# Kernel tuning notes

Measured on AMD Instinct MI355X. Metric: run time of the kernel, lower is better.

## Reference

```python
import jax, jax.numpy as jnp
import numpy as np

N, D, E, L, H, F1, G, A = 4096, 256, 131072, 3, 4, 128, 16, 32

def setup_inputs() -> dict:
    key = jax.random.key(0)
    ks = jax.random.split(key, 12)
    s = lambda k, shape, fan: jax.random.normal(k, shape, jnp.float32) / np.sqrt(fan)
    return {
        "x": jax.random.normal(ks[0], (N, D), jnp.float32),
        "edge_attr": jax.random.uniform(ks[1], (E,), jnp.float32),
        "conv_Wself": s(ks[2], (L, D, D), D),
        "conv_Wnbr": s(ks[3], (L, D, D), D),
        "conv_b": jnp.zeros((L, D), jnp.float32),
        "bn_gamma": jnp.ones((L - 1, D), jnp.float32),
        "bn_beta": jnp.zeros((L - 1, D), jnp.float32),
        "bn_mean": jnp.zeros((L - 1, D), jnp.float32),
        "bn_var": jnp.ones((L - 1, D), jnp.float32),
        "Wqkv": s(ks[4], (3, D, D), D),
        "bqkv": jnp.zeros((3, D), jnp.float32),
        "Wo": s(ks[5], (D, D), D),
        "bo": jnp.zeros((D,), jnp.float32),
        "fc1_W": s(ks[6], (D, F1), D),
        "fc1_b": jnp.zeros((F1,), jnp.float32),
        "AW1": s(ks[7], (G, F1, A), F1),
        "Ab1": jnp.zeros((G, A), jnp.float32),
        "AW2": s(ks[8], (G, A, 1), A),
        "Ab2": jnp.zeros((G, 1), jnp.float32),
        "edge_index": jax.random.randint(ks[9], (2, E), 0, N, jnp.int32),
        "node_groups": jax.random.randint(ks[10], (N,), 0, G, jnp.int32),
    }


def reference(x, edge_attr, conv_Wself, conv_Wnbr, conv_b, bn_gamma, bn_beta,
              bn_mean, bn_var, Wqkv, bqkv, Wo, bo, fc1_W, fc1_b,
              AW1, Ab1, AW2, Ab2, edge_index, node_groups):
    src, dst = edge_index[0], edge_index[1]
    # message-passing conv stack (edge_attr only used by the last, non-attention layer)
    for i in range(L):
        msg = x[src]
        if i == L - 1:
            msg = msg * edge_attr[:, None]
        agg = jax.ops.segment_sum(msg, dst, num_segments=N)
        x = x @ conv_Wself[i] + agg @ conv_Wnbr[i] + conv_b[i]
        if i < L - 1:
            x = bn_gamma[i] * (x - bn_mean[i]) * jax.lax.rsqrt(bn_var[i] + 1e-5) + bn_beta[i]
            x = jax.nn.elu(x)
    # hierarchy self-attention over all N nodes (batch of 1), residual add
    dh = D // H
    q = (x @ Wqkv[0] + bqkv[0]).reshape(N, H, dh)
    k = (x @ Wqkv[1] + bqkv[1]).reshape(N, H, dh)
    v = (x @ Wqkv[2] + bqkv[2]).reshape(N, H, dh)
    scores = jnp.einsum('nhd,mhd->hnm', q, k) / np.sqrt(dh).astype(np.float32)
    attn = jax.nn.softmax(scores, axis=-1)
    o = jnp.einsum('hnm,mhd->nhd', attn, v).reshape(N, D) @ Wo + bo
    x = x + o
    feats = jax.nn.elu(x @ fc1_W + fc1_b)  # [N, F1]; dropout is eval no-op
    # MoE-style per-node group adapter routing: gather tiny MLP weights per node
    h = jax.nn.relu(jnp.einsum('nd,nda->na', feats, AW1[node_groups]) + Ab1[node_groups])
    out = jnp.einsum('na,nao->no', h, AW2[node_groups]) + Ab2[node_groups]  # [N, 1]
    return out
```

## Files before the change

### kernel.cpp

```cpp
#include <hip/hip_runtime.h>
#include <math.h>

#define NN   4096
#define DIM  256
#define NE   131072
#define NH   4
#define DH   64
#define F1D  128
#define NG   16
#define AD   32

typedef unsigned short u16;
typedef unsigned int   u32;
typedef _Float16 f16;
typedef __attribute__((ext_vector_type(8))) _Float16 half8;
typedef __attribute__((ext_vector_type(4))) float f32x4;

enum { EPI_BIAS = 0, EPI_BNELU = 1 };
enum { MEPI_WO = 0, MEPI_FC1 = 1 };

#define MFMA16(a, b, c) __builtin_amdgcn_mfma_f32_16x16x32_f16(a, b, c, 0, 0, 0)

__device__ inline u16 f2h(float x) { union { f16 f; u16 u; } c; c.f = (f16)x; return c.u; }
__device__ inline void split16(float x, u16& h, u16& l) {
    union { f16 f; u16 u; } ch, cl;
    ch.f = (f16)x;
    cl.f = (f16)(x - (float)ch.f);
    h = ch.u; l = cl.u;
}

__global__ void csr_count(const int* __restrict__ dst, int* __restrict__ cnt) {
    int e = blockIdx.x * 256 + threadIdx.x;
    atomicAdd(&cnt[dst[e]], 1);
}

__global__ __launch_bounds__(1024) void csr_scan(
    int* __restrict__ cnt, int* __restrict__ off)
{
    __shared__ int wsum[16];
    const int t = threadIdx.x;
    const int lane = t & 63;
    int4 v = *(const int4*)&cnt[t * 4];
    const int s = v.x + v.y + v.z + v.w;
    int acc = s;
    #pragma unroll
    for (int o = 1; o < 64; o <<= 1) {
        int u = __shfl_up(acc, o);
        if (lane >= o) acc += u;
    }
    if (lane == 63) wsum[t >> 6] = acc;
    __syncthreads();
    if (t < 16) {
        int w0 = wsum[t];
        int a2 = w0;
        #pragma unroll
        for (int o = 1; o < 16; o <<= 1) {
            int u = __shfl_up(a2, o);
            if (t >= o) a2 += u;
        }
        wsum[t] = a2 - w0;
    }
    __syncthreads();
    const int base = wsum[t >> 6] + (acc - s);
    off[t * 4 + 0] = base;
    off[t * 4 + 1] = base + v.x;
    off[t * 4 + 2] = base + v.x + v.y;
    off[t * 4 + 3] = base + v.x + v.y + v.z;
    *(int4*)&cnt[t * 4] = make_int4(0, 0, 0, 0);
    if (t == 1023) off[NN] = base + s;
}

__global__ void csr_fill(const int* __restrict__ dst, const int* __restrict__ src,
                         const float* __restrict__ eattr, const int* __restrict__ off,
                         int* __restrict__ cur, int* __restrict__ esrc,
                         float* __restrict__ ewt) {
    int e = blockIdx.x * 256 + threadIdx.x;
    int d = dst[e];
    int pos = off[d] + atomicAdd(&cur[d], 1);
    esrc[pos] = src[e];
    ewt[pos]  = eattr[e];
}

__global__ __launch_bounds__(256) void prep_kernel(
    const float* __restrict__ x,
    const float* __restrict__ Ws, const float* __restrict__ Wn,
    const float* __restrict__ Wqkv, const float* __restrict__ Wo,
    const float* __restrict__ fc1W,
    u16* __restrict__ xh, u16* __restrict__ xl,
    u16* __restrict__ wch, u16* __restrict__ wcl,
    u16* __restrict__ w4h, u16* __restrict__ w4l,
    u16* __restrict__ f1h, u16* __restrict__ f1l,
    int* __restrict__ cur)
{
    const int b = blockIdx.x;
    const int t = threadIdx.x;
    if (b < 1024) {
        const int gid = b * 256 + t;
        const float4 v = *(const float4*)&x[(size_t)gid * 4];
        u16 h[4], l[4];
        split16(v.x, h[0], l[0]); split16(v.y, h[1], l[1]);
        split16(v.z, h[2], l[2]); split16(v.w, h[3], l[3]);
        *(uint2*)&xh[(size_t)gid * 4] =
            make_uint2((u32)h[0] | ((u32)h[1] << 16), (u32)h[2] | ((u32)h[3] << 16));
        *(uint2*)&xl[(size_t)gid * 4] =
            make_uint2((u32)l[0] | ((u32)l[1] << 16), (u32)l[2] | ((u32)l[3] << 16));
    } else if (b < 1408) {
        const int gid = (b - 1024) * 256 + t;
        const int L = gid / 32768;
        const int rem = gid % 32768;
        const int m = rem / 128;
        const int k4 = (rem % 128) * 4;
        const float* S = Ws + (size_t)L * 65536;
        const float* Nb = Wn + (size_t)L * 65536;
        u16 h[4], l[4];
        #pragma unroll
        for (int j = 0; j < 4; ++j) {
            const int k = k4 + j;
            const float v = (k < 256) ? S[(size_t)k * 256 + m]
                                      : Nb[(size_t)(k - 256) * 256 + m];
            split16(v, h[j], l[j]);
        }
        const size_t o = (size_t)L * 131072 + (size_t)m * 512 + k4;
        *(uint2*)&wch[o] = make_uint2((u32)h[0] | ((u32)h[1] << 16), (u32)h[2] | ((u32)h[3] << 16));
        *(uint2*)&wcl[o] = make_uint2((u32)l[0] | ((u32)l[1] << 16), (u32)l[2] | ((u32)l[3] << 16));
    } else if (b < 1664) {
        const int gid = (b - 1408) * 256 + t;
        const int mat = gid / 16384;
        const int rem = gid % 16384;
        const int m = rem / 64;
        const int k4 = (rem % 64) * 4;
        const float* W = (mat < 3) ? Wqkv + (size_t)mat * 65536 : Wo;
        u16 h[4], l[4];
        #pragma unroll
        for (int j = 0; j < 4; ++j)
            split16(W[(size_t)(k4 + j) * 256 + m], h[j], l[j]);
        const size_t o = (size_t)mat * 65536 + (size_t)m * 256 + k4;
        *(uint2*)&w4h[o] = make_uint2((u32)h[0] | ((u32)h[1] << 16), (u32)h[2] | ((u32)h[3] << 16));
        *(uint2*)&w4l[o] = make_uint2((u32)l[0] | ((u32)l[1] << 16), (u32)l[2] | ((u32)l[3] << 16));
    } else if (b < 1696) {
        const int gid = (b - 1664) * 256 + t;
        const int m = gid / 64;
        const int k4 = (gid % 64) * 4;
        u16 h[4], l[4];
        #pragma unroll
        for (int j = 0; j < 4; ++j)
            split16(fc1W[(size_t)(k4 + j) * F1D + m], h[j], l[j]);
        const size_t o = (size_t)m * 256 + k4;
        *(uint2*)&f1h[o] = make_uint2((u32)h[0] | ((u32)h[1] << 16), (u32)h[2] | ((u32)h[3] << 16));
        *(uint2*)&f1l[o] = make_uint2((u32)l[0] | ((u32)l[1] << 16), (u32)l[2] | ((u32)l[3] << 16));
    } else {
        const int gid = (b - 1696) * 256 + t;
        if (gid < NN / 4) *(int4*)&cur[gid * 4] = make_int4(0, 0, 0, 0);
    }
}

template<bool LAST>
__global__ __launch_bounds__(256) void agg_kernel(
    const float* __restrict__ x, const int* __restrict__ esrc,
    const float* __restrict__ ewt, const int* __restrict__ off,
    u16* __restrict__ aggh, u16* __restrict__ aggl)
{
    const int node = blockIdx.x * 4 + (threadIdx.x >> 6);
    const int lane = threadIdx.x & 63;
    const int d4 = lane * 4;
    int j = off[node];
    const int j1 = off[node + 1];
    float4 acc = make_float4(0.f, 0.f, 0.f, 0.f);
    for (; j + 4 <= j1; j += 4) {
        const int s0 = esrc[j], s1 = esrc[j + 1], s2 = esrc[j + 2], s3 = esrc[j + 3];
        const float4 x0 = *(const float4*)&x[(size_t)s0 * DIM + d4];
        const float4 x1 = *(const float4*)&x[(size_t)s1 * DIM + d4];
        const float4 x2 = *(const float4*)&x[(size_t)s2 * DIM + d4];
        const float4 x3 = *(const float4*)&x[(size_t)s3 * DIM + d4];
        const float w0 = LAST ? ewt[j]     : 1.f;
        const float w1 = LAST ? ewt[j + 1] : 1.f;
        const float w2 = LAST ? ewt[j + 2] : 1.f;
        const float w3 = LAST ? ewt[j + 3] : 1.f;
        acc.x = fmaf(x0.x, w0, acc.x); acc.y = fmaf(x0.y, w0, acc.y);
        acc.z = fmaf(x0.z, w0, acc.z); acc.w = fmaf(x0.w, w0, acc.w);
        acc.x = fmaf(x1.x, w1, acc.x); acc.y = fmaf(x1.y, w1, acc.y);
        acc.z = fmaf(x1.z, w1, acc.z); acc.w = fmaf(x1.w, w1, acc.w);
        acc.x = fmaf(x2.x, w2, acc.x); acc.y = fmaf(x2.y, w2, acc.y);
        acc.z = fmaf(x2.z, w2, acc.z); acc.w = fmaf(x2.w, w2, acc.w);
        acc.x = fmaf(x3.x, w3, acc.x); acc.y = fmaf(x3.y, w3, acc.y);
        acc.z = fmaf(x3.z, w3, acc.z); acc.w = fmaf(x3.w, w3, acc.w);
    }
    for (; j < j1; ++j) {
        const int s = esrc[j];
        const float w = LAST ? ewt[j] : 1.f;
        const float4 xv = *(const float4*)&x[(size_t)s * DIM + d4];
        acc.x = fmaf(xv.x, w, acc.x); acc.y = fmaf(xv.y, w, acc.y);
        acc.z = fmaf(xv.z, w, acc.z); acc.w = fmaf(xv.w, w, acc.w);
    }
    u16 h[4], l[4];
    split16(acc.x, h[0], l[0]); split16(acc.y, h[1], l[1]);
    split16(acc.z, h[2], l[2]); split16(acc.w, h[3], l[3]);
    *(uint2*)&aggh[(size_t)node * DIM + d4] =
        make_uint2((u32)h[0] | ((u32)h[1] << 16), (u32)h[2] | ((u32)h[3] << 16));
    *(uint2*)&aggl[(size_t)node * DIM + d4] =
        make_uint2((u32)l[0] | ((u32)l[1] << 16), (u32)l[2] | ((u32)l[3] << 16));
}

template<int EPI>
__global__ __launch_bounds__(256) void conv_mfma(
    const u16* __restrict__ xh, const u16* __restrict__ xl,
    const u16* __restrict__ gh, const u16* __restrict__ gl,
    const u16* __restrict__ bth, const u16* __restrict__ btl,
    const float* __restrict__ bias,
    const float* __restrict__ gamma, const float* __restrict__ beta,
    const float* __restrict__ bnmean, const float* __restrict__ bnvar,
    float* __restrict__ outf, u16* __restrict__ oh, u16* __restrict__ ol)
{
    __shared__ u16 lds[13824];
    u16* As_h = lds;
    u16* As_l = lds + 2304;
    u16* Bs_h = lds + 4608;
    u16* Bs_l = lds + 9216;
    #define TKP 72

    const int tid  = threadIdx.x;
    const int row0 = blockIdx.y * 32;
    const int col0 = blockIdx.x * 64;

    const int w   = tid >> 6;
    const int l15 = tid & 15, h4 = (tid & 63) >> 4;
    const int rh  = w & 1, ch = w >> 1;
    const int arow = tid >> 3, acs = (tid & 7) * 8;
    const int brow = tid & 63, bseg = tid >> 6;
    const int bc = bseg * 16;

    uint4 sah, sal, sbh0, sbh1, sbl0, sbl1;
    {
        sah = *((const uint4*)&xh[(size_t)(row0 + arow) * DIM + acs]);
        sal = *((const uint4*)&xl[(size_t)(row0 + arow) * DIM + acs]);
        const u16* pbh = bth + (size_t)(col0 + brow) * 512 + bc;
        const u16* pbl = btl + (size_t)(col0 + brow) * 512 + bc;
        sbh0 = ((const uint4*)pbh)[0]; sbh1 = ((const uint4*)pbh)[1];
        sbl0 = ((const uint4*)pbl)[0]; sbl1 = ((const uint4*)pbl)[1];
    }

    const f32x4 z4 = {0.f, 0.f, 0.f, 0.f};
    f32x4 acc[2] = {z4, z4};

    for (int kt = 0; kt < 8; ++kt) {
        *(uint4*)&As_h[arow * TKP + acs] = sah;
        *(uint4*)&As_l[arow * TKP + acs] = sal;
        *(uint4*)&Bs_h[brow * TKP + bc]     = sbh0;
        *(uint4*)&Bs_h[brow * TKP + bc + 8] = sbh1;
        *(uint4*)&Bs_l[brow * TKP + bc]     = sbl0;
        *(uint4*)&Bs_l[brow * TKP + bc + 8] = sbl1;
        if (kt + 1 < 8) {
            const int kn = kt + 1;
            const u16 *pah, *pal;
            if (kn < 4) {
                pah = xh + (size_t)(row0 + arow) * DIM + kn * 64 + acs;
                pal = xl + (size_t)(row0 + arow) * DIM + kn * 64 + acs;
            } else {
                pah = gh + (size_t)(row0 + arow) * DIM + (kn - 4) * 64 + acs;
                pal = gl + (size_t)(row0 + arow) * DIM + (kn - 4) * 64 + acs;
            }
            sah = *((const uint4*)pah);
            sal = *((const uint4*)pal);
            const u16* pbh = bth + (size_t)(col0 + brow) * 512 + kn * 64 + bc;
            const u16* pbl = btl + (size_t)(col0 + brow) * 512 + kn * 64 + bc;
            sbh0 = ((const uint4*)pbh)[0]; sbh1 = ((const uint4*)pbh)[1];
            sbl0 = ((const uint4*)pbl)[0]; sbl1 = ((const uint4*)pbl)[1];
        }
        __syncthreads();

        __builtin_amdgcn_s_setprio(1);
        #pragma unroll
        for (int kc = 0; kc < 2; ++kc) {
            const int dc = kc * 32 + h4 * 8;
            half8 afh, afl, bfh[2], bfl[2];
            afh = *(const half8*)&As_h[(rh * 16 + l15) * TKP + dc];
            afl = *(const half8*)&As_l[(rh * 16 + l15) * TKP + dc];
            #pragma unroll
            for (int bb = 0; bb < 2; ++bb) {
                const int r = ch * 32 + bb * 16 + l15;
                bfh[bb] = *(const half8*)&Bs_h[r * TKP + dc];
                bfl[bb] = *(const half8*)&Bs_l[r * TKP + dc];
            }
            #pragma unroll
            for (int bb = 0; bb < 2; ++bb) {
                acc[bb] = MFMA16(afh, bfh[bb], acc[bb]);
                acc[bb] = MFMA16(afh, bfl[bb], acc[bb]);
                acc[bb] = MFMA16(afl, bfh[bb], acc[bb]);
            }
        }
        __builtin_amdgcn_s_setprio(0);
        __syncthreads();
    }

    #pragma unroll
    for (int bb = 0; bb < 2; ++bb) {
        const int c  = col0 + ch * 32 + bb * 16 + l15;
        const int r0 = row0 + rh * 16 + h4 * 4;
        #pragma unroll
        for (int i = 0; i < 4; ++i) {
            const int r = r0 + i;
            float t = acc[bb][i] + bias[c];
            if (EPI == EPI_BNELU) {
                t = gamma[c] * (t - bnmean[c]) * rsqrtf(bnvar[c] + 1e-5f) + beta[c];
                t = t > 0.f ? t : expm1f(t);
            }
            outf[(size_t)r * DIM + c] = t;
            u16 hh, ll;
            split16(t, hh, ll);
            oh[(size_t)r * DIM + c] = hh;
            ol[(size_t)r * DIM + c] = ll;
        }
    }
    #undef TKP
}

__global__ __launch_bounds__(256) void qkv_mfma(
    const u16* __restrict__ xh, const u16* __restrict__ xl,
    const u16* __restrict__ wth, const u16* __restrict__ wtl,
    const float* __restrict__ bias,
    u16* __restrict__ qh_o, u16* __restrict__ ql_o,
    u16* __restrict__ kh_o, u16* __restrict__ kl_o,
    u16* __restrict__ vt_o)
{
    __shared__ u16 lds[4 * 4608];
    u16* As_h = lds;
    u16* As_l = lds + 4608;
    u16* Bs_h = lds + 9216;
    u16* Bs_l = lds + 13824;
    #define TKP 72

    const int tid  = threadIdx.x;
    const int row0 = blockIdx.y * 64;
    const int mat  = blockIdx.x >> 2;
    const int col0 = (blockIdx.x & 3) * 64;
    const float* biasp = bias + mat * DIM;

    const int w   = tid >> 6;
    const int l15 = tid & 15, h4 = (tid & 63) >> 4;
    const int rh  = w & 1, ch = w >> 1;
    const int lrow = tid & 63, lseg = tid >> 6;
    const int lc = lseg * 16;

    const size_t brow = (size_t)(mat * 256 + col0 + lrow) * 256;
    uint4 sah0, sah1, sal0, sal1, sbh0, sbh1, sbl0, sbl1;
    {
        const u16* pah = xh + (size_t)(row0 + lrow) * DIM + lc;
        const u16* pal = xl + (size_t)(row0 + lrow) * DIM + lc;
        sah0 = ((const uint4*)pah)[0]; sah1 = ((const uint4*)pah)[1];
        sal0 = ((const uint4*)pal)[0]; sal1 = ((const uint4*)pal)[1];
        sbh0 = ((const uint4*)(wth + brow + lc))[0]; sbh1 = ((const uint4*)(wth + brow + lc))[1];
        sbl0 = ((const uint4*)(wtl + brow + lc))[0]; sbl1 = ((const uint4*)(wtl + brow + lc))[1];
    }

    const f32x4 z4 = {0.f, 0.f, 0.f, 0.f};
    f32x4 acc[2][2] = {{z4, z4}, {z4, z4}};

    for (int kt = 0; kt < 4; ++kt) {
        *(uint4*)&As_h[lrow * TKP + lc]     = sah0;
        *(uint4*)&As_h[lrow * TKP + lc + 8] = sah1;
        *(uint4*)&As_l[lrow * TKP + lc]     = sal0;
        *(uint4*)&As_l[lrow * TKP + lc + 8] = sal1;
        *(uint4*)&Bs_h[lrow * TKP + lc]     = sbh0;
        *(uint4*)&Bs_h[lrow * TKP + lc + 8] = sbh1;
        *(uint4*)&Bs_l[lrow * TKP + lc]     = sbl0;
        *(uint4*)&Bs_l[lrow * TKP + lc + 8] = sbl1;
        if (kt + 1 < 4) {
            const int kb = (kt + 1) * 64 + lc;
            const u16* pah = xh + (size_t)(row0 + lrow) * DIM + kb;
            const u16* pal = xl + (size_t)(row0 + lrow) * DIM + kb;
            sah0 = ((const uint4*)pah)[0]; sah1 = ((const uint4*)pah)[1];
            sal0 = ((const uint4*)pal)[0]; sal1 = ((const uint4*)pal)[1];
            sbh0 = ((const uint4*)(wth + brow + kb))[0]; sbh1 = ((const uint4*)(wth + brow + kb))[1];
            sbl0 = ((const uint4*)(wtl + brow + kb))[0]; sbl1 = ((const uint4*)(wtl + brow + kb))[1];
        }
        __syncthreads();

        __builtin_amdgcn_s_setprio(1);
        #pragma unroll
        for (int kc = 0; kc < 2; ++kc) {
            const int dc = kc * 32 + h4 * 8;
            half8 afh[2], afl[2], bfh[2], bfl[2];
            #pragma unroll
            for (int ab = 0; ab < 2; ++ab) {
                const int r = rh * 32 + ab * 16 + l15;
                afh[ab] = *(const half8*)&As_h[r * TKP + dc];
                afl[ab] = *(const half8*)&As_l[r * TKP + dc];
            }
            #pragma unroll
            for (int bb = 0; bb < 2; ++bb) {
                const int r = ch * 32 + bb * 16 + l15;
                bfh[bb] = *(const half8*)&Bs_h[r * TKP + dc];
                bfl[bb] = *(const half8*)&Bs_l[r * TKP + dc];
            }
            #pragma unroll
            for (int ab = 0; ab < 2; ++ab)
                #pragma unroll
                for (int bb = 0; bb < 2; ++bb) {
                    acc[ab][bb] = MFMA16(afh[ab], bfh[bb], acc[ab][bb]);
                    acc[ab][bb] = MFMA16(afh[ab], bfl[bb], acc[ab][bb]);
                    acc[ab][bb] = MFMA16(afl[ab], bfh[bb], acc[ab][bb]);
                }
        }
        __builtin_amdgcn_s_setprio(0);
        __syncthreads();
    }

    const float s = (mat == 0) ? 0.125f : 1.0f;
    u16* oph = (mat == 0) ? qh_o : kh_o;
    u16* opl = (mat == 0) ? ql_o : kl_o;
    #pragma unroll
    for (int ab = 0; ab < 2; ++ab)
        #pragma unroll
        for (int bb = 0; bb < 2; ++bb) {
            const int c  = col0 + ch * 32 + bb * 16 + l15;
            const int r0 = row0 + rh * 32 + ab * 16 + h4 * 4;
            if (mat < 2) {
                #pragma unroll
                for (int i = 0; i < 4; ++i) {
                    const int r = r0 + i;
                    const float t = (acc[ab][bb][i] + biasp[c]) * s;
                    u16 hh, ll;
                    split16(t, hh, ll);
                    oph[(size_t)r * DIM + c] = hh;
                    opl[(size_t)r * DIM + c] = ll;
                }
            } else {
                u16 v[4];
                #pragma unroll
                for (int i = 0; i < 4; ++i)
                    v[i] = f2h(acc[ab][bb][i] + biasp[c]);
                *(uint2*)&vt_o[(size_t)c * NN + r0] =
                    make_uint2((u32)v[0] | ((u32)v[1] << 16), (u32)v[2] | ((u32)v[3] << 16));
            }
        }
    #undef TKP
}

template<int MEPI>
__global__ __launch_bounds__(256) void mfma_gemm(
    const u16* __restrict__ Ah, const u16* __restrict__ Al,
    const u16* __restrict__ Bth, const u16* __restrict__ Btl,
    const float* __restrict__ bias, const float* __restrict__ resid,
    float* __restrict__ outf, u16* __restrict__ outh, u16* __restrict__ outl,
    int K, int M)
{
    __shared__ u16 lds[4 * 4608];
    u16* As_h = lds;
    u16* As_l = lds + 4608;
    u16* Bs_h = lds + 9216;
    u16* Bs_l = lds + 13824;
    #define TKP 72

    const int tid  = threadIdx.x;
    const int row0 = blockIdx.y * 64;
    const int col0 = blockIdx.x * 64;

    const int w   = tid >> 6;
    const int l15 = tid & 15, h4 = (tid & 63) >> 4;
    const int rh  = w & 1, ch = w >> 1;
    const int lrow = tid & 63, lseg = tid >> 6;
    const int lc = lseg * 16;

    uint4 sah0, sah1, sal0, sal1, sbh0, sbh1, sbl0, sbl1;
    {
        const u16* pa0 = Ah  + (size_t)(row0 + lrow) * K + lc;
        const u16* pa1 = Al  + (size_t)(row0 + lrow) * K + lc;
        const u16* pb0 = Bth + (size_t)(col0 + lrow) * K + lc;
        const u16* pb1 = Btl + (size_t)(col0 + lrow) * K + lc;
        sah0 = ((const uint4*)pa0)[0]; sah1 = ((const uint4*)pa0)[1];
        sal0 = ((const uint4*)pa1)[0]; sal1 = ((const uint4*)pa1)[1];
        sbh0 = ((const uint4*)pb0)[0]; sbh1 = ((const uint4*)pb0)[1];
        sbl0 = ((const uint4*)pb1)[0]; sbl1 = ((const uint4*)pb1)[1];
    }

    const f32x4 z4 = {0.f, 0.f, 0.f, 0.f};
    f32x4 acc[2][2] = {{z4, z4}, {z4, z4}};
    const int NKT2 = K / 64;

    for (int kt = 0; kt < NKT2; ++kt) {
        *(uint4*)&As_h[lrow * TKP + lc]     = sah0;
        *(uint4*)&As_h[lrow * TKP + lc + 8] = sah1;
        *(uint4*)&As_l[lrow * TKP + lc]     = sal0;
        *(uint4*)&As_l[lrow * TKP + lc + 8] = sal1;
        *(uint4*)&Bs_h[lrow * TKP + lc]     = sbh0;
        *(uint4*)&Bs_h[lrow * TKP + lc + 8] = sbh1;
        *(uint4*)&Bs_l[lrow * TKP + lc]     = sbl0;
        *(uint4*)&Bs_l[lrow * TKP + lc + 8] = sbl1;
        if (kt + 1 < NKT2) {
            const int kb = (kt + 1) * 64 + lc;
            const u16* pa0 = Ah  + (size_t)(row0 + lrow) * K + kb;
            const u16* pa1 = Al  + (size_t)(row0 + lrow) * K + kb;
            const u16* pb0 = Bth + (size_t)(col0 + lrow) * K + kb;
            const u16* pb1 = Btl + (size_t)(col0 + lrow) * K + kb;
            sah0 = ((const uint4*)pa0)[0]; sah1 = ((const uint4*)pa0)[1];
            sal0 = ((const uint4*)pa1)[0]; sal1 = ((const uint4*)pa1)[1];
            sbh0 = ((const uint4*)pb0)[0]; sbh1 = ((const uint4*)pb0)[1];
            sbl0 = ((const uint4*)pb1)[0]; sbl1 = ((const uint4*)pb1)[1];
        }
        __syncthreads();

        __builtin_amdgcn_s_setprio(1);
        #pragma unroll
        for (int kc = 0; kc < 2; ++kc) {
            const int dc = kc * 32 + h4 * 8;
            half8 afh[2], afl[2], bfh[2], bfl[2];
            #pragma unroll
            for (int ab = 0; ab < 2; ++ab) {
                const int r = rh * 32 + ab * 16 + l15;
                afh[ab] = *(const half8*)&As_h[r * TKP + dc];
                afl[ab] = *(const half8*)&As_l[r * TKP + dc];
            }
            #pragma unroll
            for (int bb = 0; bb < 2; ++bb) {
                const int r = ch * 32 + bb * 16 + l15;
                bfh[bb] = *(const half8*)&Bs_h[r * TKP + dc];
                bfl[bb] = *(const half8*)&Bs_l[r * TKP + dc];
            }
            #pragma unroll
            for (int ab = 0; ab < 2; ++ab)
                #pragma unroll
                for (int bb = 0; bb < 2; ++bb) {
                    acc[ab][bb] = MFMA16(afh[ab], bfh[bb], acc[ab][bb]);
                    acc[ab][bb] = MFMA16(afh[ab], bfl[bb], acc[ab][bb]);
                    acc[ab][bb] = MFMA16(afl[ab], bfh[bb], acc[ab][bb]);
                }
        }
        __builtin_amdgcn_s_setprio(0);
        __syncthreads();
    }

    #pragma unroll
    for (int ab = 0; ab < 2; ++ab)
        #pragma unroll
        for (int bb = 0; bb < 2; ++bb) {
            const int c  = col0 + ch * 32 + bb * 16 + l15;
            const int r0 = row0 + rh * 32 + ab * 16 + h4 * 4;
            #pragma unroll
            for (int i = 0; i < 4; ++i) {
                const int r = r0 + i;
                float t = acc[ab][bb][i] + bias[c];
                if (MEPI == MEPI_WO) {
                    t += resid[(size_t)r * M + c];
                    u16 hh, ll;
                    split16(t, hh, ll);
                    outh[(size_t)r * M + c] = hh;
                    outl[(size_t)r * M + c] = ll;
                } else {
                    t = t > 0.f ? t : expm1f(t);
                    outf[(size_t)r * M + c] = t;
                }
            }
        }
    #undef TKP
}

#define QB 128
#define KB 64
#define NSPLIT 4
#define NKT (NN / KB)
#define KP 72

__global__ __launch_bounds__(512, 2) void attn_kernel(
    const u16* __restrict__ qhi, const u16* __restrict__ qlo,
    const u16* __restrict__ khi, const u16* __restrict__ klo,
    const u16* __restrict__ vT,
    float* __restrict__ op0, float* __restrict__ op1,
    float* __restrict__ op2, float* __restrict__ op3,
    float* __restrict__ mpart, float* __restrict__ lpart)
{
    __shared__ u16 lds[37120];
    u16* Kh0 = lds;
    u16* Kl0 = lds + 4608;
    u16* Vt0 = lds + 9216;
    u16* Kh1 = lds + 13824;
    u16* Kl1 = lds + 18432;
    u16* Vt1 = lds + 23040;
    u16* Pb  = lds + 27648;
    u16* Qh  = lds;
    u16* Ql  = lds + 13824;
    float* frow = (float*)(lds + 36864);

    const int tid = threadIdx.x;
    const int h   = blockIdx.y;
    const int q0  = blockIdx.x * QB;
    const int sp  = blockIdx.z;
    const int kt0 = sp * (NKT / NSPLIT);
    const int kt1 = kt0 + NKT / NSPLIT;

    const int w   = tid >> 6;
    const int l15 = tid & 15, h4 = (tid & 63) >> 4;
    const int lrow = tid & 63, lseg = tid >> 6;
    const int gq8 = h * DH + lseg * 8;

    {
        const int qrow = tid >> 2, qseg = tid & 3;
        const u16* s0 = qhi + (size_t)(q0 + qrow) * DIM + h * DH + qseg * 16;
        const u16* s1 = qlo + (size_t)(q0 + qrow) * DIM + h * DH + qseg * 16;
        uint4 a = ((const uint4*)s0)[0], b = ((const uint4*)s0)[1];
        uint4 c = ((const uint4*)s1)[0], d = ((const uint4*)s1)[1];
        *(uint4*)&Qh[qrow * KP + qseg * 16]     = a;
        *(uint4*)&Qh[qrow * KP + qseg * 16 + 8] = b;
        *(uint4*)&Ql[qrow * KP + qseg * 16]     = c;
        *(uint4*)&Ql[qrow * KP + qseg * 16 + 8] = d;
    }

    uint4 rk, rl, rv;
    auto load_tile = [&](int kt_ld) {
        const int key0 = kt_ld * KB;
        rk = *(const uint4*)(khi + (size_t)(key0 + lrow) * DIM + gq8);
        rl = *(const uint4*)(klo + (size_t)(key0 + lrow) * DIM + gq8);
        rv = *(const uint4*)(vT + (size_t)(h * DH + lrow) * NN + key0 + lseg * 8);
    };
    load_tile(kt0);
    __syncthreads();

    half8 qf[2][2];
    #pragma unroll
    for (int kc = 0; kc < 2; ++kc) {
        const int r = w * 16 + l15;
        const int dc = kc * 32 + h4 * 8;
        qf[kc][0] = *(const half8*)&Qh[r * KP + dc];
        qf[kc][1] = *(const half8*)&Ql[r * KP + dc];
    }
    __syncthreads();

    auto stage_to = [&](u16* Kh, u16* Kl, u16* Vt) {
        *(uint4*)&Kh[lrow * KP + lseg * 8] = rk;
        *(uint4*)&Kl[lrow * KP + lseg * 8] = rl;
        *(uint4*)&Vt[lrow * KP + lseg * 8] = rv;
    };

    stage_to(Kh0, Kl0, Vt0);
    load_tile(kt0 + 1);
    __syncthreads();

    const f32x4 z4 = {0.f, 0.f, 0.f, 0.f};
    f32x4 oacc[4] = {z4, z4, z4, z4};
    float m_run[4], l_run[4];
    #pragma unroll
    for (int i = 0; i < 4; ++i) { m_run[i] = -3.0e38f; l_run[i] = 0.f; }

    auto tile_body = [&](int t, u16* Kc, u16* Lc, u16* Vc,
                         u16* Kn, u16* Ln, u16* Vn) {
        if (t + 1 < kt1) stage_to(Kn, Ln, Vn);
        if (t + 2 < kt1) load_tile(t + 2);

        f32x4 sc[4] = {z4, z4, z4, z4};
        __builtin_amdgcn_s_setprio(1);
        #pragma unroll
        for (int kc = 0; kc < 2; ++kc) {
            const int dc = kc * 32 + h4 * 8;
            half8 kfh[4], kfl[4];
            #pragma unroll
            for (int kcb = 0; kcb < 4; ++kcb) {
                const int r = kcb * 16 + l15;
                kfh[kcb] = *(const half8*)&Kc[r * KP + dc];
                kfl[kcb] = *(const half8*)&Lc[r * KP + dc];
            }
            #pragma unroll
            for (int kcb = 0; kcb < 4; ++kcb) {
                sc[kcb] = MFMA16(qf[kc][0], kfh[kcb], sc[kcb]);
                sc[kcb] = MFMA16(qf[kc][0], kfl[kcb], sc[kcb]);
                sc[kcb] = MFMA16(qf[kc][1], kfh[kcb], sc[kcb]);
            }
        }
        __builtin_amdgcn_s_setprio(0);
        float p[4][4], fr[4];
        #pragma unroll
        for (int i = 0; i < 4; ++i) {
            float pm = fmaxf(fmaxf(sc[0][i], sc[1][i]), fmaxf(sc[2][i], sc[3][i]));
            #pragma unroll
            for (int off = 1; off < 16; off <<= 1)
                pm = fmaxf(pm, __shfl_xor(pm, off));
            const float mnew = fmaxf(m_run[i], pm);
            fr[i] = __expf(m_run[i] - mnew);
            m_run[i] = mnew;
            p[0][i] = __expf(sc[0][i] - mnew);
            p[1][i] = __expf(sc[1][i] - mnew);
            p[2][i] = __expf(sc[2][i] - mnew);
            p[3][i] = __expf(sc[3][i] - mnew);
            float ls = (p[0][i] + p[1][i]) + (p[2][i] + p[3][i]);
            #pragma unroll
            for (int off = 1; off < 16; off <<= 1) ls += __shfl_xor(ls, off);
            l_run[i] = l_run[i] * fr[i] + ls;
        }
        #pragma unroll
        for (int kcb = 0; kcb < 4; ++kcb) {
            const int kk = kcb * 16 + l15;
            #pragma unroll
            for (int i = 0; i < 4; ++i)
                Pb[(w * 16 + h4 * 4 + i) * KP + kk] = f2h(p[kcb][i]);
        }
        if (l15 == 0) {
            #pragma unroll
            for (int i = 0; i < 4; ++i)
                frow[w * 16 + h4 * 4 + i] = fr[i];
        }
        const float frq = frow[w * 16 + l15];
        #pragma unroll
        for (int db = 0; db < 4; ++db) oacc[db] *= frq;
        __builtin_amdgcn_s_setprio(1);
        #pragma unroll
        for (int kc = 0; kc < 2; ++kc) {
            const half8 pf = *(const half8*)&Pb[(w * 16 + l15) * KP + kc * 32 + h4 * 8];
            #pragma unroll
            for (int db = 0; db < 4; ++db) {
                const half8 vf = *(const half8*)&Vc[(db * 16 + l15) * KP + kc * 32 + h4 * 8];
                oacc[db] = MFMA16(vf, pf, oacc[db]);
            }
        }
        __builtin_amdgcn_s_setprio(0);
        __syncthreads();
    };

    for (int t = kt0; t < kt1; t += 2) {
        tile_body(t,     Kh0, Kl0, Vt0, Kh1, Kl1, Vt1);
        tile_body(t + 1, Kh1, Kl1, Vt1, Kh0, Kl0, Vt0);
    }

    float* ob = (sp == 0) ? op0 : ((sp == 1) ? op1 : ((sp == 2) ? op2 : op3));
    #pragma unroll
    for (int db = 0; db < 4; ++db)
        *(f32x4*)&ob[(size_t)(q0 + w * 16 + l15) * DIM + h * DH + db * 16 + h4 * 4] = oacc[db];
    if (l15 == 0) {
        #pragma unroll
        for (int i = 0; i < 4; ++i) {
            const int r = w * 16 + h4 * 4 + i;
            mpart[((size_t)sp * NN + q0 + r) * NH + h] = m_run[i];
            lpart[((size_t)sp * NN + q0 + r) * NH + h] = l_run[i];
        }
    }
}

__global__ __launch_bounds__(256) void attn_combine(
    const float* __restrict__ o0, const float* __restrict__ o1,
    const float* __restrict__ o2, const float* __restrict__ o3,
    const float* __restrict__ mp, const float* __restrict__ lp,
    u16* __restrict__ ohi, u16* __restrict__ olo)
{
    const int gid = blockIdx.x * 256 + threadIdx.x;
    const int row = gid >> 6;
    const int c4  = (gid & 63) * 4;
    const int h   = c4 >> 6;
    float m[4], wgt[4];
    #pragma unroll
    for (int z = 0; z < 4; ++z) m[z] = mp[((size_t)z * NN + row) * NH + h];
    const float M = fmaxf(fmaxf(m[0], m[1]), fmaxf(m[2], m[3]));
    float den = 0.f;
    #pragma unroll
    for (int z = 0; z < 4; ++z) {
        wgt[z] = __expf(m[z] - M);
        den += lp[((size_t)z * NN + row) * NH + h] * wgt[z];
    }
    const float inv = 1.f / den;
    const float4 a = *(const float4*)&o0[(size_t)row * DIM + c4];
    const float4 b = *(const float4*)&o1[(size_t)row * DIM + c4];
    const float4 c = *(const float4*)&o2[(size_t)row * DIM + c4];
    const float4 d = *(const float4*)&o3[(size_t)row * DIM + c4];
    float r[4];
    r[0] = (a.x * wgt[0] + b.x * wgt[1] + c.x * wgt[2] + d.x * wgt[3]) * inv;
    r[1] = (a.y * wgt[0] + b.y * wgt[1] + c.y * wgt[2] + d.y * wgt[3]) * inv;
    r[2] = (a.z * wgt[0] + b.z * wgt[1] + c.z * wgt[2] + d.z * wgt[3]) * inv;
    r[3] = (a.w * wgt[0] + b.w * wgt[1] + c.w * wgt[2] + d.w * wgt[3]) * inv;
    u16 hh[4], ll[4];
    #pragma unroll
    for (int j = 0; j < 4; ++j) split16(r[j], hh[j], ll[j]);
    *(uint2*)&ohi[(size_t)row * DIM + c4] =
        make_uint2((u32)hh[0] | ((u32)hh[1] << 16), (u32)hh[2] | ((u32)hh[3] << 16));
    *(uint2*)&olo[(size_t)row * DIM + c4] =
        make_uint2((u32)ll[0] | ((u32)ll[1] << 16), (u32)ll[2] | ((u32)ll[3] << 16));
}

__global__ __launch_bounds__(64) void adapter_kernel(
    const float* __restrict__ feats, const int* __restrict__ grp,
    const float* __restrict__ AW1, const float* __restrict__ Ab1,
    const float* __restrict__ AW2, const float* __restrict__ Ab2,
    float* __restrict__ out)
{
    const int n = blockIdx.x;
    const int lane = threadIdx.x;
    __shared__ float f[F1D];
    f[lane]      = feats[(size_t)n * F1D + lane];
    f[lane + 64] = feats[(size_t)n * F1D + 64 + lane];
    __syncthreads();
    const int g = grp[n];
    const float* W1 = AW1 + (size_t)g * F1D * AD;
    const int a = lane & 31;
    const int half = lane >> 5;
    float hsum = 0.f;
    for (int d = 0; d < 64; ++d)
        hsum = fmaf(f[half * 64 + d], W1[(half * 64 + d) * AD + a], hsum);
    hsum += __shfl_xor(hsum, 32);
    hsum = fmaxf(hsum + Ab1[g * AD + a], 0.f);
    float p = hsum * AW2[g * AD + a];
    #pragma unroll
    for (int mm = 1; mm < 32; mm <<= 1) p += __shfl_xor(p, mm);
    if (lane == 0) out[n] = p + Ab2[g];
}

extern "C" void kernel_launch(void* const* d_in, const int* in_sizes, int n_in,
                              void* d_out, int out_size, void* d_ws, size_t ws_size,
                              hipStream_t stream)
{
    const float* x_in   = (const float*)d_in[0];
    const float* eattr  = (const float*)d_in[1];
    const float* Wself  = (const float*)d_in[2];
    const float* Wnbr   = (const float*)d_in[3];
    const float* convb  = (const float*)d_in[4];
    const float* gamma  = (const float*)d_in[5];
    const float* beta   = (const float*)d_in[6];
    const float* bnmean = (const float*)d_in[7];
    const float* bnvar  = (const float*)d_in[8];
    const float* Wqkv   = (const float*)d_in[9];
    const float* bqkv   = (const float*)d_in[10];
    const float* Wo     = (const float*)d_in[11];
    const float* bo     = (const float*)d_in[12];
    const float* fc1W   = (const float*)d_in[13];
    const float* fc1b   = (const float*)d_in[14];
    const float* AW1    = (const float*)d_in[15];
    const float* Ab1    = (const float*)d_in[16];
    const float* AW2    = (const float*)d_in[17];
    const float* Ab2    = (const float*)d_in[18];
    const int*   eidx   = (const int*)d_in[19];
    const int*   grp    = (const int*)d_in[20];
    const int* srcArr = eidx;
    const int* dstArr = eidx + NE;

    float* fws = (float*)d_ws;
    const size_t NM = (size_t)NN * DIM;
    float* bufA  = fws;
    float* bufB  = fws + NM;
    float* bufC  = fws + 2 * NM;
    float* feats = fws + 3 * NM;
    float* mpart = fws + 3 * NM + NM / 2;
    float* lpart = mpart + 4 * NN * NH;
    u16* up = (u16*)(lpart + 4 * NN * NH);
    u16* xpAh = up;             u16* xpAl = xpAh + NM;
    u16* xpBh = xpAl + NM;      u16* xpBl = xpBh + NM;
    u16* aggh = xpBl + NM;      u16* aggl = aggh + NM;
    u16* qh = aggl + NM;        u16* ql = qh + NM;
    u16* kh = ql + NM;          u16* kl = kh + NM;
    u16* vt = kl + NM;
    u16* wcath = vt + NM;
    u16* wcatl = wcath + 3 * 131072;
    u16* wt4h  = wcatl + 3 * 131072;
    u16* wt4l  = wt4h + 4 * 65536;
    u16* fc1h  = wt4l + 4 * 65536;
    u16* fc1l  = fc1h + 32768;
    int*   esrc = (int*)(fc1l + 32768);
    float* ewt  = (float*)(esrc + NE);
    int* off    = (int*)(ewt + NE);
    int* cur    = off + NN + 1;
    float* outp = (float*)d_out;

    float* op2 = (float*)xpAh;
    float* op3 = (float*)xpBh;

    prep_kernel<<<1700, 256, 0, stream>>>(
        x_in, Wself, Wnbr, Wqkv, Wo, fc1W,
        xpAh, xpAl, wcath, wcatl, wt4h, wt4l, fc1h, fc1l, cur);

    csr_count<<<NE / 256, 256, 0, stream>>>(dstArr, cur);
    csr_scan<<<1, 1024, 0, stream>>>(cur, off);
    csr_fill<<<NE / 256, 256, 0, stream>>>(dstArr, srcArr, eattr, off, cur, esrc, ewt);

    const dim3 gc(DIM / 64, NN / 32);
    const int rgrid = NN * DIM / 4 / 256;

    agg_kernel<false><<<NN / 4, 256, 0, stream>>>(x_in, esrc, ewt, off, aggh, aggl);
    conv_mfma<EPI_BNELU><<<gc, 256, 0, stream>>>(
        xpAh, xpAl, aggh, aggl, wcath, wcatl, convb,
        gamma, beta, bnmean, bnvar, bufA, xpBh, xpBl);
    agg_kernel<false><<<NN / 4, 256, 0, stream>>>(bufA, esrc, ewt, off, aggh, aggl);
    conv_mfma<EPI_BNELU><<<gc, 256, 0, stream>>>(
        xpBh, xpBl, aggh, aggl, wcath + 131072, wcatl + 131072, convb + DIM,
        gamma + DIM, beta + DIM, bnmean + DIM, bnvar + DIM, bufC, xpAh, xpAl);
    agg_kernel<true><<<NN / 4, 256, 0, stream>>>(bufC, esrc, ewt, off, aggh, aggl);
    conv_mfma<EPI_BIAS><<<gc, 256, 0, stream>>>(
        xpAh, xpAl, aggh, aggl, wcath + 262144, wcatl + 262144, convb + 2 * DIM,
        nullptr, nullptr, nullptr, nullptr, bufA, xpBh, xpBl);

    qkv_mfma<<<dim3(12, NN / 64), 256, 0, stream>>>(
        xpBh, xpBl, wt4h, wt4l, bqkv, qh, ql, kh, kl, vt);

    attn_kernel<<<dim3(NN / QB, NH, NSPLIT), 512, 0, stream>>>(
        qh, ql, kh, kl, vt, bufB, bufC, op2, op3, mpart, lpart);
    attn_combine<<<rgrid, 256, 0, stream>>>(
        bufB, bufC, op2, op3, mpart, lpart, qh, ql);

    mfma_gemm<MEPI_WO><<<dim3(DIM / 64, NN / 64), 256, 0, stream>>>(
        qh, ql, wt4h + 3 * 65536, wt4l + 3 * 65536, bo, bufA,
        nullptr, kh, kl, DIM, DIM);

    mfma_gemm<MEPI_FC1><<<dim3(F1D / 64, NN / 64), 256, 0, stream>>>(
        kh, kl, fc1h, fc1l, fc1b, nullptr, feats, nullptr, nullptr, DIM, F1D);

    adapter_kernel<<<NN, 64, 0, stream>>>(feats, grp, AW1, Ab1, AW2, Ab2, outp);
}
```

Before: 237.1 us.

## Shrink GEMM tiles, single-buffer attention with lazy rescale, batch adapter nodes

The Wo and fc1 GEMMs now use 32-row tiles, which doubles the number of blocks for better CU fill. The attention kernel drops double-buffered K/V staging to cut LDS so three blocks fit per CU. It also skips the running-max rescale of the output accumulator unless a new row max exceeds the old one by more than 8. The adapter kernel processes four nodes per 256-thread block instead of one per 64-thread block. The tradeoffs are less load/compute overlap in attention, and relying on a bounded exponent growth for fp16 P values in the no-rescale path.

Result: slower. 248.4 us (+4.7%).

```diff
diff --git a/kernel.cpp b/kernel.cpp
--- a/kernel.cpp
+++ b/kernel.cpp
@@ -437,65 +437,60 @@
 }
 
 template<int MEPI>
-__global__ __launch_bounds__(256) void mfma_gemm(
+__global__ __launch_bounds__(256) void mfma_gemm32(
     const u16* __restrict__ Ah, const u16* __restrict__ Al,
     const u16* __restrict__ Bth, const u16* __restrict__ Btl,
     const float* __restrict__ bias, const float* __restrict__ resid,
     float* __restrict__ outf, u16* __restrict__ outh, u16* __restrict__ outl,
     int K, int M)
 {
-    __shared__ u16 lds[4 * 4608];
+    __shared__ u16 lds[13824];
     u16* As_h = lds;
-    u16* As_l = lds + 4608;
-    u16* Bs_h = lds + 9216;
-    u16* Bs_l = lds + 13824;
+    u16* As_l = lds + 2304;
+    u16* Bs_h = lds + 4608;
+    u16* Bs_l = lds + 9216;
     #define TKP 72
 
     const int tid  = threadIdx.x;
-    const int row0 = blockIdx.y * 64;
+    const int row0 = blockIdx.y * 32;
     const int col0 = blockIdx.x * 64;
 
     const int w   = tid >> 6;
     const int l15 = tid & 15, h4 = (tid & 63) >> 4;
     const int rh  = w & 1, ch = w >> 1;
-    const int lrow = tid & 63, lseg = tid >> 6;
-    const int lc = lseg * 16;
-
-    uint4 sah0, sah1, sal0, sal1, sbh0, sbh1, sbl0, sbl1;
+    const int arow = tid >> 3, acs = (tid & 7) * 8;
+    const int brow = tid & 63, bseg = tid >> 6;
+    const int bc = bseg * 16;
+
+    uint4 sah, sal, sbh0, sbh1, sbl0, sbl1;
     {
-        const u16* pa0 = Ah  + (size_t)(row0 + lrow) * K + lc;
-        const u16* pa1 = Al  + (size_t)(row0 + lrow) * K + lc;
-        const u16* pb0 = Bth + (size_t)(col0 + lrow) * K + lc;
-        const u16* pb1 = Btl + (size_t)(col0 + lrow) * K + lc;
-        sah0 = ((const uint4*)pa0)[0]; sah1 = ((const uint4*)pa0)[1];
-        sal0 = ((const uint4*)pa1)[0]; sal1 = ((const uint4*)pa1)[1];
-        sbh0 = ((const uint4*)pb0)[0]; sbh1 = ((const uint4*)pb0)[1];
-        sbl0 = ((const uint4*)pb1)[0]; sbl1 = ((const uint4*)pb1)[1];
+        sah = *((const uint4*)&Ah[(size_t)(row0 + arow) * K + acs]);
+        sal = *((const uint4*)&Al[(size_t)(row0 + arow) * K + acs]);
+        const u16* pbh = Bth + (size_t)(col0 + brow) * K + bc;
+        const u16* pbl = Btl + (size_t)(col0 + brow) * K + bc;
+        sbh0 = ((const uint4*)pbh)[0]; sbh1 = ((const uint4*)pbh)[1];
+        sbl0 = ((const uint4*)pbl)[0]; sbl1 = ((const uint4*)pbl)[1];
     }
 
     const f32x4 z4 = {0.f, 0.f, 0.f, 0.f};
-    f32x4 acc[2][2] = {{z4, z4}, {z4, z4}};
+    f32x4 acc[2] = {z4, z4};
     const int NKT2 = K / 64;
 
     for (int kt = 0; kt < NKT2; ++kt) {
-        *(uint4*)&As_h[lrow * TKP + lc]     = sah0;
-        *(uint4*)&As_h[lrow * TKP + lc + 8] = sah1;
-        *(uint4*)&As_l[lrow * TKP + lc]     = sal0;
-        *(uint4*)&As_l[lrow * TKP + lc + 8] = sal1;
-        *(uint4*)&Bs_h[lrow * TKP + lc]     = sbh0;
-        *(uint4*)&Bs_h[lrow * TKP + lc + 8] = sbh1;
-        *(uint4*)&Bs_l[lrow * TKP + lc]     = sbl0;
-        *(uint4*)&Bs_l[lrow * TKP + lc + 8] = sbl1;
+        *(uint4*)&As_h[arow * TKP + acs] = sah;
+        *(uint4*)&As_l[arow * TKP + acs] = sal;
+        *(uint4*)&Bs_h[brow * TKP + bc]     = sbh0;
+        *(uint4*)&Bs_h[brow * TKP + bc + 8] = sbh1;
+        *(uint4*)&Bs_l[brow * TKP + bc]     = sbl0;
+        *(uint4*)&Bs_l[brow * TKP + bc + 8] = sbl1;
         if (kt + 1 < NKT2) {
-            const int kb = (kt + 1) * 64 + lc;
-            const u16* pa0 = Ah  + (size_t)(row0 + lrow) * K + kb;
-            const u16* pa1 = Al  + (size_t)(row0 + lrow) * K + kb;
-            const u16* pb0 = Bth + (size_t)(col0 + lrow) * K + kb;
-            const u16* pb1 = Btl + (size_t)(col0 + lrow) * K + kb;
-            sah0 = ((const uint4*)pa0)[0]; sah1 = ((const uint4*)pa0)[1];
-            sal0 = ((const uint4*)pa1)[0]; sal1 = ((const uint4*)pa1)[1];
-            sbh0 = ((const uint4*)pb0)[0]; sbh1 = ((const uint4*)pb0)[1];
-            sbl0 = ((const uint4*)pb1)[0]; sbl1 = ((const uint4*)pb1)[1];
+            const int kb = (kt + 1) * 64;
+            sah = *((const uint4*)&Ah[(size_t)(row0 + arow) * K + kb + acs]);
+            sal = *((const uint4*)&Al[(size_t)(row0 + arow) * K + kb + acs]);
+            const u16* pbh = Bth + (size_t)(col0 + brow) * K + kb + bc;
+            const u16* pbl = Btl + (size_t)(col0 + brow) * K + kb + bc;
+            sbh0 = ((const uint4*)pbh)[0]; sbh1 = ((const uint4*)pbh)[1];
+            sbl0 = ((const uint4*)pbl)[0]; sbl1 = ((const uint4*)pbl)[1];
         }
         __syncthreads();
 
@@ -503,13 +498,9 @@
         #pragma unroll
         for (int kc = 0; kc < 2; ++kc) {
             const int dc = kc * 32 + h4 * 8;
-            half8 afh[2], afl[2], bfh[2], bfl[2];
-            #pragma unroll
-            for (int ab = 0; ab < 2; ++ab) {
-                const int r = rh * 32 + ab * 16 + l15;
-                afh[ab] = *(const half8*)&As_h[r * TKP + dc];
-                afl[ab] = *(const half8*)&As_l[r * TKP + dc];
-            }
+            half8 afh, afl, bfh[2], bfl[2];
+            afh = *(const half8*)&As_h[(rh * 16 + l15) * TKP + dc];
+            afl = *(const half8*)&As_l[(rh * 16 + l15) * TKP + dc];
             #pragma unroll
             for (int bb = 0; bb < 2; ++bb) {
                 const int r = ch * 32 + bb * 16 + l15;
@@ -517,40 +508,36 @@
                 bfl[bb] = *(const half8*)&Bs_l[r * TKP + dc];
             }
             #pragma unroll
-            for (int ab = 0; ab < 2; ++ab)
-                #pragma unroll
-                for (int bb = 0; bb < 2; ++bb) {
-                    acc[ab][bb] = MFMA16(afh[ab], bfh[bb], acc[ab][bb]);
-                    acc[ab][bb] = MFMA16(afh[ab], bfl[bb], acc[ab][bb]);
-                    acc[ab][bb] = MFMA16(afl[ab], bfh[bb], acc[ab][bb]);
-                }
+            for (int bb = 0; bb < 2; ++bb) {
+                acc[bb] = MFMA16(afh, bfh[bb], acc[bb]);
+                acc[bb] = MFMA16(afh, bfl[bb], acc[bb]);
+                acc[bb] = MFMA16(afl, bfh[bb], acc[bb]);
+            }
         }
         __builtin_amdgcn_s_setprio(0);
         __syncthreads();
     }
 
     #pragma unroll
-    for (int ab = 0; ab < 2; ++ab)
-        #pragma unroll
-        for (int bb = 0; bb < 2; ++bb) {
-            const int c  = col0 + ch * 32 + bb * 16 + l15;
-            const int r0 = row0 + rh * 32 + ab * 16 + h4 * 4;
-            #pragma unroll
-            for (int i = 0; i < 4; ++i) {
-                const int r = r0 + i;
-                float t = acc[ab][bb][i] + bias[c];
-                if (MEPI == MEPI_WO) {
-                    t += resid[(size_t)r * M + c];
-                    u16 hh, ll;
-                    split16(t, hh, ll);
-                    outh[(size_t)r * M + c] = hh;
-                    outl[(size_t)r * M + c] = ll;
-                } else {
-                    t = t > 0.f ? t : expm1f(t);
-                    outf[(size_t)r * M + c] = t;
-                }
-            }
-        }
+    for (int bb = 0; bb < 2; ++bb) {
+        const int c  = col0 + ch * 32 + bb * 16 + l15;
+        const int r0 = row0 + rh * 16 + h4 * 4;
+        #pragma unroll
+        for (int i = 0; i < 4; ++i) {
+            const int r = r0 + i;
+            float t = acc[bb][i] + bias[c];
+            if (MEPI == MEPI_WO) {
+                t += resid[(size_t)r * M + c];
+                u16 hh, ll;
+                split16(t, hh, ll);
+                outh[(size_t)r * M + c] = hh;
+                outl[(size_t)r * M + c] = ll;
+            } else {
+                t = t > 0.f ? t : expm1f(t);
+                outf[(size_t)r * M + c] = t;
+            }
+        }
+    }
     #undef TKP
 }
 
@@ -560,7 +547,7 @@
 #define NKT (NN / KB)
 #define KP 72
 
-__global__ __launch_bounds__(512, 2) void attn_kernel(
+__global__ __launch_bounds__(512, 3) void attn_kernel(
     const u16* __restrict__ qhi, const u16* __restrict__ qlo,
     const u16* __restrict__ khi, const u16* __restrict__ klo,
     const u16* __restrict__ vT,
@@ -568,17 +555,14 @@
     float* __restrict__ op2, float* __restrict__ op3,
     float* __restrict__ mpart, float* __restrict__ lpart)
 {
-    __shared__ u16 lds[37120];
-    u16* Kh0 = lds;
-    u16* Kl0 = lds + 4608;
-    u16* Vt0 = lds + 9216;
-    u16* Kh1 = lds + 13824;
-    u16* Kl1 = lds + 18432;
-    u16* Vt1 = lds + 23040;
-    u16* Pb  = lds + 27648;
-    u16* Qh  = lds;
-    u16* Ql  = lds + 13824;
-    float* frow = (float*)(lds + 36864);
+    __shared__ u16 lds[23296];
+    u16* Kh = lds;
+    u16* Kl = lds + 4608;
+    u16* Vt = lds + 9216;
+    u16* Pb = lds + 13824;
+    u16* Qh = lds;
+    u16* Ql = lds + 9216;
+    float* frow = (float*)(lds + 23040);
 
     const int tid = threadIdx.x;
     const int h   = blockIdx.y;
@@ -624,26 +608,18 @@
     }
     __syncthreads();
 
-    auto stage_to = [&](u16* Kh, u16* Kl, u16* Vt) {
+    const f32x4 z4 = {0.f, 0.f, 0.f, 0.f};
+    f32x4 oacc[4] = {z4, z4, z4, z4};
+    float m_run[4], l_run[4];
+    #pragma unroll
+    for (int i = 0; i < 4; ++i) { m_run[i] = -3.0e38f; l_run[i] = 0.f; }
+
+    for (int t = kt0; t < kt1; ++t) {
         *(uint4*)&Kh[lrow * KP + lseg * 8] = rk;
         *(uint4*)&Kl[lrow * KP + lseg * 8] = rl;
         *(uint4*)&Vt[lrow * KP + lseg * 8] = rv;
-    };
-
-    stage_to(Kh0, Kl0, Vt0);
-    load_tile(kt0 + 1);
-    __syncthreads();
-
-    const f32x4 z4 = {0.f, 0.f, 0.f, 0.f};
-    f32x4 oacc[4] = {z4, z4, z4, z4};
-    float m_run[4], l_run[4];
-    #pragma unroll
-    for (int i = 0; i < 4; ++i) { m_run[i] = -3.0e38f; l_run[i] = 0.f; }
-
-    auto tile_body = [&](int t, u16* Kc, u16* Lc, u16* Vc,
-                         u16* Kn, u16* Ln, u16* Vn) {
-        if (t + 1 < kt1) stage_to(Kn, Ln, Vn);
-        if (t + 2 < kt1) load_tile(t + 2);
+        if (t + 1 < kt1) load_tile(t + 1);
+        __syncthreads();
 
         f32x4 sc[4] = {z4, z4, z4, z4};
         __builtin_amdgcn_s_setprio(1);
@@ -654,8 +630,8 @@
             #pragma unroll
             for (int kcb = 0; kcb < 4; ++kcb) {
                 const int r = kcb * 16 + l15;
-                kfh[kcb] = *(const half8*)&Kc[r * KP + dc];
-                kfl[kcb] = *(const half8*)&Lc[r * KP + dc];
+                kfh[kcb] = *(const half8*)&Kh[r * KP + dc];
+                kfl[kcb] = *(const half8*)&Kl[r * KP + dc];
             }
             #pragma unroll
             for (int kcb = 0; kcb < 4; ++kcb) {
@@ -665,24 +641,55 @@
             }
         }
         __builtin_amdgcn_s_setprio(0);
-        float p[4][4], fr[4];
+
+        float pm[4];
         #pragma unroll
         for (int i = 0; i < 4; ++i) {
-            float pm = fmaxf(fmaxf(sc[0][i], sc[1][i]), fmaxf(sc[2][i], sc[3][i]));
+            float v = fmaxf(fmaxf(sc[0][i], sc[1][i]), fmaxf(sc[2][i], sc[3][i]));
             #pragma unroll
             for (int off = 1; off < 16; off <<= 1)
-                pm = fmaxf(pm, __shfl_xor(pm, off));
-            const float mnew = fmaxf(m_run[i], pm);
-            fr[i] = __expf(m_run[i] - mnew);
-            m_run[i] = mnew;
-            p[0][i] = __expf(sc[0][i] - mnew);
-            p[1][i] = __expf(sc[1][i] - mnew);
-            p[2][i] = __expf(sc[2][i] - mnew);
-            p[3][i] = __expf(sc[3][i] - mnew);
-            float ls = (p[0][i] + p[1][i]) + (p[2][i] + p[3][i]);
-            #pragma unroll
-            for (int off = 1; off < 16; off <<= 1) ls += __shfl_xor(ls, off);
-            l_run[i] = l_run[i] * fr[i] + ls;
+                v = fmaxf(v, __shfl_xor(v, off));
+            pm[i] = v;
+        }
+        const int ok = (pm[0] - m_run[0] <= 8.f) && (pm[1] - m_run[1] <= 8.f) &&
+                       (pm[2] - m_run[2] <= 8.f) && (pm[3] - m_run[3] <= 8.f);
+        float p[4][4];
+        if (__all(ok)) {
+            #pragma unroll
+            for (int i = 0; i < 4; ++i) {
+                p[0][i] = __expf(sc[0][i] - m_run[i]);
+                p[1][i] = __expf(sc[1][i] - m_run[i]);
+                p[2][i] = __expf(sc[2][i] - m_run[i]);
+                p[3][i] = __expf(sc[3][i] - m_run[i]);
+                float ls = (p[0][i] + p[1][i]) + (p[2][i] + p[3][i]);
+                #pragma unroll
+                for (int off = 1; off < 16; off <<= 1) ls += __shfl_xor(ls, off);
+                l_run[i] += ls;
+            }
+        } else {
+            float fr[4];
+            #pragma unroll
+            for (int i = 0; i < 4; ++i) {
+                const float mnew = fmaxf(m_run[i], pm[i]);
+                fr[i] = __expf(m_run[i] - mnew);
+                m_run[i] = mnew;
+                p[0][i] = __expf(sc[0][i] - mnew);
+                p[1][i] = __expf(sc[1][i] - mnew);
+                p[2][i] = __expf(sc[2][i] - mnew);
+                p[3][i] = __expf(sc[3][i] - mnew);
+                float ls = (p[0][i] + p[1][i]) + (p[2][i] + p[3][i]);
+                #pragma unroll
+                for (int off = 1; off < 16; off <<= 1) ls += __shfl_xor(ls, off);
+                l_run[i] = l_run[i] * fr[i] + ls;
+            }
+            if (l15 == 0) {
+                #pragma unroll
+                for (int i = 0; i < 4; ++i)
+                    frow[w * 16 + h4 * 4 + i] = fr[i];
+            }
+            const float frq = frow[w * 16 + l15];
+            #pragma unroll
+            for (int db = 0; db < 4; ++db) oacc[db] *= frq;
         }
         #pragma unroll
         for (int kcb = 0; kcb < 4; ++kcb) {
@@ -691,31 +698,18 @@
             for (int i = 0; i < 4; ++i)
                 Pb[(w * 16 + h4 * 4 + i) * KP + kk] = f2h(p[kcb][i]);
         }
-        if (l15 == 0) {
-            #pragma unroll
-            for (int i = 0; i < 4; ++i)
-                frow[w * 16 + h4 * 4 + i] = fr[i];
-        }
-        const float frq = frow[w * 16 + l15];
-        #pragma unroll
-        for (int db = 0; db < 4; ++db) oacc[db] *= frq;
         __builtin_amdgcn_s_setprio(1);
         #pragma unroll
         for (int kc = 0; kc < 2; ++kc) {
             const half8 pf = *(const half8*)&Pb[(w * 16 + l15) * KP + kc * 32 + h4 * 8];
             #pragma unroll
             for (int db = 0; db < 4; ++db) {
-                const half8 vf = *(const half8*)&Vc[(db * 16 + l15) * KP + kc * 32 + h4 * 8];
+                const half8 vf = *(const half8*)&Vt[(db * 16 + l15) * KP + kc * 32 + h4 * 8];
                 oacc[db] = MFMA16(vf, pf, oacc[db]);
             }
         }
         __builtin_amdgcn_s_setprio(0);
         __syncthreads();
-    };
-
-    for (int t = kt0; t < kt1; t += 2) {
-        tile_body(t,     Kh0, Kl0, Vt0, Kh1, Kl1, Vt1);
-        tile_body(t + 1, Kh1, Kl1, Vt1, Kh0, Kl0, Vt0);
     }
 
     float* ob = (sp == 0) ? op0 : ((sp == 1) ? op1 : ((sp == 2) ? op2 : op3));
@@ -771,25 +765,25 @@
         make_uint2((u32)ll[0] | ((u32)ll[1] << 16), (u32)ll[2] | ((u32)ll[3] << 16));
 }
 
-__global__ __launch_bounds__(64) void adapter_kernel(
+__global__ __launch_bounds__(256) void adapter_kernel(
     const float* __restrict__ feats, const int* __restrict__ grp,
     const float* __restrict__ AW1, const float* __restrict__ Ab1,
     const float* __restrict__ AW2, const float* __restrict__ Ab2,
     float* __restrict__ out)
 {
-    const int n = blockIdx.x;
-    const int lane = threadIdx.x;
-    __shared__ float f[F1D];
-    f[lane]      = feats[(size_t)n * F1D + lane];
-    f[lane + 64] = feats[(size_t)n * F1D + 64 + lane];
-    __syncthreads();
+    const int wv = threadIdx.x >> 6;
+    const int n = blockIdx.x * 4 + wv;
+    const int lane = threadIdx.x & 63;
+    __shared__ float f[4][F1D];
+    f[wv][lane]      = feats[(size_t)n * F1D + lane];
+    f[wv][lane + 64] = feats[(size_t)n * F1D + 64 + lane];
     const int g = grp[n];
     const float* W1 = AW1 + (size_t)g * F1D * AD;
     const int a = lane & 31;
     const int half = lane >> 5;
     float hsum = 0.f;
     for (int d = 0; d < 64; ++d)
-        hsum = fmaf(f[half * 64 + d], W1[(half * 64 + d) * AD + a], hsum);
+        hsum = fmaf(f[wv][half * 64 + d], W1[(half * 64 + d) * AD + a], hsum);
     hsum += __shfl_xor(hsum, 32);
     hsum = fmaxf(hsum + Ab1[g * AD + a], 0.f);
     float p = hsum * AW2[g * AD + a];
@@ -888,12 +882,12 @@
     attn_combine<<<rgrid, 256, 0, stream>>>(
         bufB, bufC, op2, op3, mpart, lpart, qh, ql);
 
-    mfma_gemm<MEPI_WO><<<dim3(DIM / 64, NN / 64), 256, 0, stream>>>(
+    mfma_gemm32<MEPI_WO><<<dim3(DIM / 64, NN / 32), 256, 0, stream>>>(
         qh, ql, wt4h + 3 * 65536, wt4l + 3 * 65536, bo, bufA,
         nullptr, kh, kl, DIM, DIM);
 
-    mfma_gemm<MEPI_FC1><<<dim3(F1D / 64, NN / 64), 256, 0, stream>>>(
+    mfma_gemm32<MEPI_FC1><<<dim3(F1D / 64, NN / 32), 256, 0, stream>>>(
         kh, kl, fc1h, fc1l, fc1b, nullptr, feats, nullptr, nullptr, DIM, F1D);
 
-    adapter_kernel<<<NN, 64, 0, stream>>>(feats, grp, AW1, Ab1, AW2, Ab2, outp);
-}
+    adapter_kernel<<<NN / 4, 256, 0, stream>>>(feats, grp, AW1, Ab1, AW2, Ab2, outp);
+}
```
